# Kernel optimization log

Measured on AMD Instinct MI355X. Metric: run time of the kernel, lower is better.

Reference implementation:

```python
import jax, jax.numpy as jnp
import numpy as np

K_NEIGHBORS = 50
DELTA = 0.001


def setup_inputs() -> dict:
    key = jax.random.key(0)
    k1, k2, k3 = jax.random.split(key, 3)
    A, N, D, B = 8, 50000, 64, 256
    return {
        "query": jax.random.normal(k1, (B, D), dtype=jnp.float32),
        "mem_keys": jax.random.normal(k2, (A, N, D), dtype=jnp.float32),
        "mem_values": jax.random.normal(k3, (A, N), dtype=jnp.float32),
    }


def reference(query, mem_keys, mem_values):
    # query: [B, D]; mem_keys: [A, N, D]; mem_values: [A, N]
    q_sq = jnp.sum(query ** 2, axis=-1, keepdims=True)  # [B, 1]

    def per_action(keys, values):
        # keys: [N, D], values: [N]
        # brute-force squared-L2 distances (replaces Annoy ANN search)
        d2 = q_sq + jnp.sum(keys ** 2, axis=-1)[None, :] - 2.0 * query @ keys.T  # [B, N]
        _, idx = jax.lax.top_k(-d2, K_NEIGHBORS)  # [B, K] nearest indices
        gk = keys[idx]        # [B, K, D] gathered keys
        gv = values[idx]      # [B, K]    gathered values
        # inverse-distance kernel, exact recompute as in torch forward
        dist = jnp.sum((query[:, None, :] - gk) ** 2, axis=-1)  # [B, K]
        w = 1.0 / (dist + DELTA)
        out = jnp.sum(w * gv, axis=-1) / jnp.sum(w, axis=-1)  # [B]
        return out, idx, dist

    vals, idxs, scores = jax.vmap(per_action)(mem_keys, mem_values)  # [A,B], [A,B,K], [A,B,K]
    values_all = vals.T  # [B, A]
    max_values = jnp.max(values_all, axis=-1, keepdims=True)   # [B, 1]
    actions = jnp.argmax(values_all, axis=-1, keepdims=True)   # [B, 1]
    return (max_values, actions, values_all,
            jnp.transpose(idxs, (1, 0, 2)), jnp.transpose(scores, (1, 0, 2)))
```

## Files before the change

kernel.cpp:

```cpp
#include <hip/hip_runtime.h>
#include <cstdint>


#define A_N 8
#define N_N 50000
#define D_N 64
#define B_N 256
#define K_N 50

constexpr int   QT  = 64;
constexpr int   NBT = 128;
constexpr int   NT  = (N_N + NBT - 1) / NBT;
constexpr int   SL  = 56;
constexpr int   SLF = 64;
constexpr int   SLOTS = 20;
constexpr int   CAPMAX = 4096;
constexpr float TMARG = 25.0f;
constexpr int   NPAD = NT * NBT;

constexpr int OFF_MAX = 0;
constexpr int OFF_ACT = 256;
constexpr int OFF_VAL = 512;
constexpr int OFF_IDX = 2560;
constexpr int OFF_SC  = 104960;

constexpr size_t WSF_CNT  = 0;
constexpr size_t WSF_THR  = 8192;
constexpr size_t WSF_KBF  = 1609728;
constexpr size_t WSF_CAND = 52858880;

constexpr size_t WS_CNT  = 0;
constexpr size_t WS_QSQ  = 16384;
constexpr size_t WS_KSQ  = 17408;
constexpr size_t WS_CAND = 1617920;

typedef __attribute__((ext_vector_type(8))) short bf16x8;
typedef __attribute__((ext_vector_type(4))) float f32x4;

__device__ __forceinline__ unsigned bfr(float f)
{
    unsigned u = __float_as_uint(f);
    return (u + 0x7FFFu + ((u >> 16) & 1u)) >> 16;
}
__device__ __forceinline__ uint4 packbf8(const float* f)
{
    uint4 w;
    w.x = bfr(f[0]) | (bfr(f[1]) << 16);
    w.y = bfr(f[2]) | (bfr(f[3]) << 16);
    w.z = bfr(f[4]) | (bfr(f[5]) << 16);
    w.w = bfr(f[6]) | (bfr(f[7]) << 16);
    return w;
}

__device__ __forceinline__ void async16(void* lds, const void* g)
{
    __builtin_amdgcn_global_load_lds(
        (const __attribute__((address_space(1))) void*)g,
        (__attribute__((address_space(3))) void*)lds, 16, 0, 0);
}

__device__ __forceinline__ float np_tree8(const float r[8])
{
    return __fadd_rn(__fadd_rn(__fadd_rn(r[0], r[1]), __fadd_rn(r[2], r[3])),
                     __fadd_rn(__fadd_rn(r[4], r[5]), __fadd_rn(r[6], r[7])));
}

__device__ __forceinline__ float np_sumsq64(const float* __restrict__ a)
{
    float r[8];
#pragma unroll
    for (int j = 0; j < 8; ++j) r[j] = __fmul_rn(a[j], a[j]);
    for (int i = 8; i < 64; i += 8)
#pragma unroll
        for (int j = 0; j < 8; ++j)
            r[j] = __fadd_rn(r[j], __fmul_rn(a[i + j], a[i + j]));
    return np_tree8(r);
}

__device__ __forceinline__ float np_sum50(const float* __restrict__ a)
{
    float r[8];
#pragma unroll
    for (int j = 0; j < 8; ++j) r[j] = a[j];
    for (int i = 8; i < 48; i += 8)
#pragma unroll
        for (int j = 0; j < 8; ++j) r[j] = __fadd_rn(r[j], a[i + j]);
    float res = np_tree8(r);
    res = __fadd_rn(res, a[48]);
    res = __fadd_rn(res, a[49]);
    return res;
}


__global__ __launch_bounds__(256)
void dnd_k0b(const float* __restrict__ keys, float* __restrict__ thrn,
             uint4* __restrict__ kbf, int* __restrict__ cnt)
{
    __shared__ float khalf[NBT][2];
    const int t   = blockIdx.x;
    const int a   = blockIdx.y;
    const int tid = threadIdx.x;
    const int r   = tid >> 1, h = tid & 1;

    int n = t * NBT + r; if (n > N_N - 1) n = N_N - 1;
    const float4* s4 = (const float4*)(keys + ((size_t)a * N_N + n) * D_N + h * 32);
    float4 fv[8];
#pragma unroll
    for (int i = 0; i < 8; ++i) fv[i] = s4[i];
    float ps = 0.f;
#pragma unroll
    for (int i = 0; i < 8; ++i)
        ps += fv[i].x * fv[i].x + fv[i].y * fv[i].y + fv[i].z * fv[i].z + fv[i].w * fv[i].w;
    khalf[r][h] = ps;

    const float* f = (const float*)fv;
    const int s = r >> 4, m = r & 15;
    uint4* dst = kbf + ((size_t)(a * NT + t) * 16 + (s * 2 + h)) * 64;
#pragma unroll
    for (int g = 0; g < 4; ++g) dst[g * 16 + m] = packbf8(f + g * 8);

    __syncthreads();
    if (tid < NBT) {
        const int nn = t * NBT + tid;
        float thr = __builtin_huge_valf();
        if (nn < N_N) {
            const float ks = khalf[tid][0] + khalf[tid][1];
            thr = 0.5f * (ks - TMARG);
        }
        thrn[(size_t)a * NPAD + t * NBT + tid] = thr;
    }
    if (t == 0) cnt[a * B_N + tid] = 0;
}

__global__ __launch_bounds__(256, 7)
void dnd_k1(const float* __restrict__ query, const uint4* __restrict__ kbf,
            const float* __restrict__ thrn,
            int* __restrict__ cnt, unsigned* __restrict__ cand, int cap)
{
    __shared__ __align__(16) uint4 bfrag[16][64];
    __shared__ float    thrs[NBT];
    __shared__ int      lcnt[QT];
    __shared__ unsigned lbuf[QT][SLOTS];

    const int a    = blockIdx.z;
    const int q0   = blockIdx.y * QT;
    const int sl   = blockIdx.x;
    const int tid  = threadIdx.x;
    const int lane = tid & 63;
    const int wave = tid >> 6;
    const int quad = lane >> 4;
    const int nl   = lane & 15;

    bf16x8 aA, aB;
    {
        const float* qb = query + (size_t)(q0 + wave * 16 + nl) * D_N + quad * 8;
        float f0[8], f1[8];
        *(float4*)(f0)     = *(const float4*)(qb);
        *(float4*)(f0 + 4) = *(const float4*)(qb + 4);
        *(float4*)(f1)     = *(const float4*)(qb + 32);
        *(float4*)(f1 + 4) = *(const float4*)(qb + 36);
        uint4 pa = packbf8(f0), pb = packbf8(f1);
        aA = *(bf16x8*)&pa;
        aB = *(bf16x8*)&pb;
    }
    if (tid < QT) lcnt[tid] = 0;

    int it = 0;
    for (int t = sl; t < NT; t += SL, ++it) {
        const int n0 = t * NBT;
        __syncthreads();
        {
            const char* src = (const char*)(kbf + (size_t)(a * NT + t) * 1024);
#pragma unroll
            for (int i = 0; i < 4; ++i) {
                const int off = i * 4096 + tid * 16;
                async16((char*)bfrag + off, src + off);
            }
        }
        if (tid < NBT) thrs[tid] = thrn[(size_t)a * NPAD + n0 + tid];
        __syncthreads();

#pragma unroll
        for (int s = 0; s < 8; ++s) {
            const bf16x8 b0 = ((const bf16x8*)bfrag)[(s * 2 + 0) * 64 + lane];
            const bf16x8 b1 = ((const bf16x8*)bfrag)[(s * 2 + 1) * 64 + lane];
            f32x4 c = {0.f, 0.f, 0.f, 0.f};
            c = __builtin_amdgcn_mfma_f32_16x16x32_bf16(aA, b0, c, 0, 0, 0);
            c = __builtin_amdgcn_mfma_f32_16x16x32_bf16(aB, b1, c, 0, 0, 0);

            const int   nn  = n0 + s * 16 + nl;
            const float thr = thrs[s * 16 + nl];
#pragma unroll
            for (int r = 0; r < 4; ++r) {
                if (c[r] >= thr) {
                    const int bl = wave * 16 + quad * 4 + r;
                    const float d2rel = fmaf(-2.f, c[r], fmaf(2.f, thr, TMARG));
                    int qv = (int)fmaf(d2rel, 1000.f, 40000.f);
                    qv = qv < 0 ? 0 : (qv > 65535 ? 65535 : qv);
                    const unsigned entry = ((unsigned)qv << 16) | (unsigned)nn;
                    const int p = atomicAdd(&lcnt[bl], 1);
                    if (p < SLOTS) lbuf[bl][p] = entry;
                    else {
                        const int gb = a * B_N + q0 + bl;
                        const int gp = atomicAdd(&cnt[gb], 1);
                        if (gp < cap) cand[(size_t)gb * cap + gp] = entry;
                    }
                }
            }
        }

        const bool last = (t + SL >= NT);
        if ((it & 1) || last) {
            __syncthreads();
            if (tid < QT) {
                int m = lcnt[tid]; lcnt[tid] = 0;
                if (m > SLOTS) m = SLOTS;
                if (m > 0) {
                    const int gb = a * B_N + q0 + tid;
                    const int base = atomicAdd(&cnt[gb], m);
                    unsigned* dst = cand + (size_t)gb * cap;
                    for (int i = 0; i < m; ++i) {
                        const int p = base + i;
                        if (p < cap) dst[p] = lbuf[tid][i];
                    }
                }
            }
        }
    }
}

__global__ __launch_bounds__(256)
void dnd_k2(const float* __restrict__ query, const float* __restrict__ keys,
            const float* __restrict__ values,
            const int* __restrict__ cnt, const unsigned* __restrict__ cand, int cap,
            float* __restrict__ dout)
{
    __shared__ __align__(16) float qrow[D_N];
    __shared__ int   hist[256];
    __shared__ float sdf[512];
    __shared__ int   sn[512];
    __shared__ int   wn[K_N];
    __shared__ float wsc[K_N];
    __shared__ float wgv[K_N];
    __shared__ int   nsurv;
    __shared__ int   bstar;
    __shared__ float qsq_np;

    const int b   = blockIdx.x;
    const int a   = blockIdx.y;
    const int ab  = a * B_N + b;
    const int tid = threadIdx.x;

    if (tid < D_N) qrow[tid] = query[(size_t)b * D_N + tid];
    hist[tid & 255] = 0;
    if (tid == 0) nsurv = 0;
    if (tid < K_N) wn[tid] = 0;
    __syncthreads();
    if (tid == 0) qsq_np = np_sumsq64(qrow);
    __syncthreads();

    int c = cnt[ab]; if (c > cap) c = cap;
    const unsigned* base = cand + (size_t)ab * cap;

    for (int i = tid; i < c; i += 256) {
        int bin = (int)(base[i] >> 16) / 250;
        bin = bin > 255 ? 255 : bin;
        atomicAdd(&hist[bin], 1);
    }
    __syncthreads();
    if (tid == 0) {
        const int need = c < K_N ? c : K_N;
        int cum = 0, bs = 255;
        for (int i = 0; i < 256; ++i) { cum += hist[i]; if (cum >= need) { bs = i; break; } }
        bstar = bs;
    }
    __syncthreads();
    const int bs = bstar + 4;

    for (int i = tid; i < c; i += 256) {
        const unsigned e = base[i];
        int bin = (int)(e >> 16) / 250;
        bin = bin > 255 ? 255 : bin;
        if (bin <= bs) {
            int p = atomicAdd(&nsurv, 1);
            if (p < 512) sn[p] = (int)(e & 0xFFFFu);
        }
    }
    __syncthreads();
    int c2 = nsurv; if (c2 > 512) c2 = 512;

    const float qn = qsq_np;
    for (int i = tid; i < c2; i += 256) {
        const int n = sn[i];
        const float4* kr = (const float4*)(keys + ((size_t)a * N_N + n) * D_N);
        const float4* qr = (const float4*)qrow;
        float r[8];
#pragma unroll
    for (int j = 0; j < 8; ++j) r[j] = 0.f;
        float dot = 0.f;
#pragma unroll
        for (int cch = 0; cch < 16; ++cch) {
            float4 kk = kr[cch]; float4 qv = qr[cch];
            const int j0 = (cch & 1) * 4;
            if (cch < 2) {
                r[j0 + 0] = __fmul_rn(kk.x, kk.x);
                r[j0 + 1] = __fmul_rn(kk.y, kk.y);
                r[j0 + 2] = __fmul_rn(kk.z, kk.z);
                r[j0 + 3] = __fmul_rn(kk.w, kk.w);
            } else {
                r[j0 + 0] = __fadd_rn(r[j0 + 0], __fmul_rn(kk.x, kk.x));
                r[j0 + 1] = __fadd_rn(r[j0 + 1], __fmul_rn(kk.y, kk.y));
                r[j0 + 2] = __fadd_rn(r[j0 + 2], __fmul_rn(kk.z, kk.z));
                r[j0 + 3] = __fadd_rn(r[j0 + 3], __fmul_rn(kk.w, kk.w));
            }
            dot = __fmaf_rn(qv.x, kk.x, dot);
            dot = __fmaf_rn(qv.y, kk.y, dot);
            dot = __fmaf_rn(qv.z, kk.z, dot);
            dot = __fmaf_rn(qv.w, kk.w, dot);
        }
        const float ksq = np_tree8(r);
        sdf[i] = __fsub_rn(__fadd_rn(qn, ksq), __fmul_rn(2.0f, dot));
    }
    __syncthreads();

    for (int i = tid; i < c2; i += 256) {
        const float di = sdf[i]; const int ni = sn[i];
        int rank = 0;
        for (int j = 0; j < c2; ++j) {
            const float dj = sdf[j]; const int nj = sn[j];
            rank += (dj < di || (dj == di && nj < ni)) ? 1 : 0;
        }
        if (rank < K_N) wn[rank] = ni;
    }
    __syncthreads();

    if (tid < K_N) {
        const int n = wn[tid];
        const float* kr = keys + ((size_t)a * N_N + n) * D_N;
        float r[8];
#pragma unroll
        for (int j = 0; j < 8; ++j) {
            float d = __fsub_rn(qrow[j], kr[j]);
            r[j] = __fmul_rn(d, d);
        }
        for (int i = 8; i < 64; i += 8)
#pragma unroll
            for (int j = 0; j < 8; ++j) {
                float d = __fsub_rn(qrow[i + j], kr[i + j]);
                r[j] = __fadd_rn(r[j], __fmul_rn(d, d));
            }
        const float dist = np_tree8(r);
        wsc[tid] = dist;
        wgv[tid] = values[(size_t)a * N_N + n];
        dout[OFF_IDX + (size_t)(b * A_N + a) * K_N + tid] = (float)n;
        dout[OFF_SC  + (size_t)(b * A_N + a) * K_N + tid] = dist;
    }
    __syncthreads();

    if (tid == 0) {
        float w[K_N], wv[K_N];
#pragma unroll
        for (int k = 0; k < K_N; ++k) {
            w[k]  = __fdiv_rn(1.0f, __fadd_rn(wsc[k], 0.001f));
            wv[k] = __fmul_rn(w[k], wgv[k]);
        }
        dout[OFF_VAL + b * A_N + a] = __fdiv_rn(np_sum50(wv), np_sum50(w));
    }
}

__global__ void dnd_k3(float* __restrict__ dout)
{
    const int b = threadIdx.x;
    float best = -__builtin_huge_valf(); int bi = 0;
#pragma unroll
    for (int a = 0; a < A_N; ++a) {
        const float v = dout[OFF_VAL + b * A_N + a];
        if (v > best) { best = v; bi = a; }
    }
    dout[OFF_MAX + b] = best;
    dout[OFF_ACT + b] = (float)bi;
}


__global__ __launch_bounds__(256)
void dnd_k0f(const float* __restrict__ query, const float* __restrict__ keys,
             float* __restrict__ qsq_g, float* __restrict__ ksq_g)
{
    const int r = blockIdx.x * 256 + threadIdx.x;
    if (r >= A_N * N_N + B_N) return;
    const bool isk = r < A_N * N_N;
    const float4* s4 = (const float4*)(isk ? (keys + (size_t)r * D_N)
                                           : (query + (size_t)(r - A_N * N_N) * D_N));
    float s = 0.f;
#pragma unroll
    for (int i = 0; i < 16; ++i) {
        float4 v = s4[i];
        s += v.x * v.x + v.y * v.y + v.z * v.z + v.w * v.w;
    }
    if (isk) ksq_g[r] = s; else qsq_g[r - A_N * N_N] = s;
}

__global__ __launch_bounds__(256, 4)
void dnd_k1f(const float* __restrict__ query, const float* __restrict__ keys,
             const float* __restrict__ qsq_g, const float* __restrict__ ksq_g,
             int* __restrict__ cnt, uint2* __restrict__ cand, int cap)
{
    __shared__ __align__(16) uint4 afrag[4][2][64];
    __shared__ __align__(16) uint4 bfrag[8][2][64];
    __shared__ float qsqs[QT];
    __shared__ float ksqs[NBT];

    const int a    = blockIdx.z;
    const int q0   = blockIdx.y * QT;
    const int sl   = blockIdx.x;
    const int tid  = threadIdx.x;
    const int lane = tid & 63;
    const int wave = tid >> 6;
    const int quad = lane >> 4;
    const int nl   = lane & 15;

    {
        const int r = tid & 63, seg = tid >> 6;
        const float4* s4 = (const float4*)(query + (size_t)(q0 + r) * D_N + seg * 16);
        float4 fv[4];
#pragma unroll
        for (int i = 0; i < 4; ++i) fv[i] = s4[i];
        const float* f = (const float*)fv;
        const int qtile = r >> 4, m = r & 15, kh = seg >> 1;
        const int quadA = (seg & 1) * 2;
        afrag[qtile][kh][quadA * 16 + m]       = packbf8(f);
        afrag[qtile][kh][(quadA + 1) * 16 + m] = packbf8(f + 8);
    }
    if (tid < QT) qsqs[tid] = qsq_g[q0 + tid];

    for (int t = sl; t < NT; t += SLF) {
        const int n0 = t * NBT;
        __syncthreads();
        {
            const int r = tid >> 1, h = tid & 1;
            int n = n0 + r; if (n > N_N - 1) n = N_N - 1;
            const float4* s4 = (const float4*)(keys + ((size_t)a * N_N + n) * D_N + h * 32);
            float4 fv[8];
#pragma unroll
            for (int i = 0; i < 8; ++i) fv[i] = s4[i];
            const float* f = (const float*)fv;
            const int s = r >> 4, m = r & 15;
#pragma unroll
            for (int g = 0; g < 4; ++g)
                bfrag[s][h][g * 16 + m] = packbf8(f + g * 8);
        }
        if (tid < NBT)
            ksqs[tid] = (n0 + tid < N_N) ? ksq_g[(size_t)a * N_N + n0 + tid]
                                         : __builtin_huge_valf();
        __syncthreads();

        const bf16x8 aA = ((const bf16x8*)afrag)[(wave * 2 + 0) * 64 + lane];
        const bf16x8 aB = ((const bf16x8*)afrag)[(wave * 2 + 1) * 64 + lane];

#pragma unroll
        for (int s = 0; s < 8; ++s) {
            const bf16x8 b0 = ((const bf16x8*)bfrag)[(s * 2 + 0) * 64 + lane];
            const bf16x8 b1 = ((const bf16x8*)bfrag)[(s * 2 + 1) * 64 + lane];
            f32x4 c = {0.f, 0.f, 0.f, 0.f};
            c = __builtin_amdgcn_mfma_f32_16x16x32_bf16(aA, b0, c, 0, 0, 0);
            c = __builtin_amdgcn_mfma_f32_16x16x32_bf16(aB, b1, c, 0, 0, 0);

            const int   nn  = n0 + s * 16 + nl;
            const float ksq = ksqs[s * 16 + nl];
#pragma unroll
            for (int r = 0; r < 4; ++r) {
                const int   qr = wave * 16 + quad * 4 + r;
                const float qq = qsqs[qr];
                const float d2 = qq + ksq - 2.0f * c[r];
                if (d2 <= qq + TMARG) {
                    const int b = q0 + qr;
                    const int p = atomicAdd(&cnt[a * B_N + b], 1);
                    if (p < cap) {
                        uint2 e; e.x = __float_as_uint(d2); e.y = (unsigned)nn;
                        cand[(size_t)(a * B_N + b) * cap + p] = e;
                    }
                }
            }
        }
    }
}

__global__ __launch_bounds__(256, 2)
void dnd_k2f(const float* __restrict__ query, const float* __restrict__ keys,
             const float* __restrict__ values,
             const int* __restrict__ cnt, const uint2* __restrict__ cand, int cap,
             float* __restrict__ dout)
{
    __shared__ __align__(16) float qrow[D_N];
    __shared__ float cd[CAPMAX];
    __shared__ int   cn[CAPMAX];
    __shared__ int   hist[256];
    __shared__ float sdf[512];
    __shared__ int   sn[512];
    __shared__ int   wn[K_N];
    __shared__ float wsc[K_N];
    __shared__ float wgv[K_N];
    __shared__ int   nsurv;
    __shared__ int   bstar;
    __shared__ float sqsq;
    __shared__ float qsq_np;

    const int b   = blockIdx.x;
    const int a   = blockIdx.y;
    const int ab  = a * B_N + b;
    const int tid = threadIdx.x;

    if (tid < D_N) qrow[tid] = query[(size_t)b * D_N + tid];
    hist[tid & 255] = 0;
    if (tid == 0) nsurv = 0;
    if (tid < K_N) wn[tid] = 0;
    __syncthreads();
    if (tid < 64) {
        float v = qrow[tid];
        float s = v * v;
#pragma unroll
        for (int m = 1; m < 64; m <<= 1) s += __shfl_xor(s, m, 64);
        if (tid == 0) sqsq = s;
    }
    if (tid == 0) qsq_np = np_sumsq64(qrow);
    __syncthreads();

    int c = cnt[ab]; if (c > cap) c = cap; if (c > CAPMAX) c = CAPMAX;
    const float qq = sqsq;

    for (int i = tid; i < c; i += 256) {
        uint2 e = cand[(size_t)ab * cap + i];
        float d = __uint_as_float(e.x);
        cd[i] = d; cn[i] = (int)e.y;
        int bin = (int)((d - qq + 40.f) * 4.f);
        bin = bin < 0 ? 0 : (bin > 255 ? 255 : bin);
        atomicAdd(&hist[bin], 1);
    }
    __syncthreads();
    if (tid == 0) {
        const int need = c < K_N ? c : K_N;
        int cum = 0, bs = 255;
        for (int i = 0; i < 256; ++i) { cum += hist[i]; if (cum >= need) { bs = i; break; } }
        bstar = bs;
    }
    __syncthreads();
    const int bs = bstar + 4;

    for (int i = tid; i < c; i += 256) {
        float d = cd[i];
        int bin = (int)((d - qq + 40.f) * 4.f);
        bin = bin < 0 ? 0 : (bin > 255 ? 255 : bin);
        if (bin <= bs) {
            int p = atomicAdd(&nsurv, 1);
            if (p < 512) sn[p] = cn[i];
        }
    }
    __syncthreads();
    int c2 = nsurv; if (c2 > 512) c2 = 512;

    const float qn = qsq_np;
    for (int i = tid; i < c2; i += 256) {
        const int n = sn[i];
        const float4* kr = (const float4*)(keys + ((size_t)a * N_N + n) * D_N);
        const float4* qr = (const float4*)qrow;
        float r[8];
#pragma unroll
        for (int j = 0; j < 8; ++j) r[j] = 0.f;
        float dot = 0.f;
#pragma unroll
        for (int cch = 0; cch < 16; ++cch) {
            float4 kk = kr[cch]; float4 qv = qr[cch];
            const int j0 = (cch & 1) * 4;
            if (cch < 2) {
                r[j0 + 0] = __fmul_rn(kk.x, kk.x);
                r[j0 + 1] = __fmul_rn(kk.y, kk.y);
                r[j0 + 2] = __fmul_rn(kk.z, kk.z);
                r[j0 + 3] = __fmul_rn(kk.w, kk.w);
            } else {
                r[j0 + 0] = __fadd_rn(r[j0 + 0], __fmul_rn(kk.x, kk.x));
                r[j0 + 1] = __fadd_rn(r[j0 + 1], __fmul_rn(kk.y, kk.y));
                r[j0 + 2] = __fadd_rn(r[j0 + 2], __fmul_rn(kk.z, kk.z));
                r[j0 + 3] = __fadd_rn(r[j0 + 3], __fmul_rn(kk.w, kk.w));
            }
            dot = __fmaf_rn(qv.x, kk.x, dot);
            dot = __fmaf_rn(qv.y, kk.y, dot);
            dot = __fmaf_rn(qv.z, kk.z, dot);
            dot = __fmaf_rn(qv.w, kk.w, dot);
        }
        const float ksq = np_tree8(r);
        sdf[i] = __fsub_rn(__fadd_rn(qn, ksq), __fmul_rn(2.0f, dot));
    }
    __syncthreads();

    for (int i = tid; i < c2; i += 256) {
        const float di = sdf[i]; const int ni = sn[i];
        int rank = 0;
        for (int j = 0; j < c2; ++j) {
            const float dj = sdf[j]; const int nj = sn[j];
            rank += (dj < di || (dj == di && nj < ni)) ? 1 : 0;
        }
        if (rank < K_N) wn[rank] = ni;
    }
    __syncthreads();

    if (tid < K_N) {
        const int n = wn[tid];
        const float* kr = keys + ((size_t)a * N_N + n) * D_N;
        float r[8];
#pragma unroll
        for (int j = 0; j < 8; ++j) {
            float d = __fsub_rn(qrow[j], kr[j]);
            r[j] = __fmul_rn(d, d);
        }
        for (int i = 8; i < 64; i += 8)
#pragma unroll
            for (int j = 0; j < 8; ++j) {
                float d = __fsub_rn(qrow[i + j], kr[i + j]);
                r[j] = __fadd_rn(r[j], __fmul_rn(d, d));
            }
        const float dist = np_tree8(r);
        wsc[tid] = dist;
        wgv[tid] = values[(size_t)a * N_N + n];
        dout[OFF_IDX + (size_t)(b * A_N + a) * K_N + tid] = (float)n;
        dout[OFF_SC  + (size_t)(b * A_N + a) * K_N + tid] = dist;
    }
    __syncthreads();

    if (tid == 0) {
        float w[K_N], wv[K_N];
#pragma unroll
        for (int k = 0; k < K_N; ++k) {
            w[k]  = __fdiv_rn(1.0f, __fadd_rn(wsc[k], 0.001f));
            wv[k] = __fmul_rn(w[k], wgv[k]);
        }
        dout[OFF_VAL + b * A_N + a] = __fdiv_rn(np_sum50(wv), np_sum50(w));
    }
}

extern "C" void kernel_launch(void* const* d_in, const int* in_sizes, int n_in,
                              void* d_out, int out_size, void* d_ws, size_t ws_size,
                              hipStream_t stream)
{
    (void)in_sizes; (void)n_in; (void)out_size;
    const float* query  = (const float*)d_in[0];
    const float* keys   = (const float*)d_in[1];
    const float* values = (const float*)d_in[2];
    float* dout = (float*)d_out;
    char*  ws   = (char*)d_ws;

    long long capf = 0;
    if (ws_size > WSF_CAND)
        capf = (long long)((ws_size - WSF_CAND) / ((size_t)A_N * B_N * 4));
    const bool full = capf >= 3072;

    if (full) {
        int cap = capf > CAPMAX ? CAPMAX : (int)capf;
        int*      cnt  = (int*)(ws + WSF_CNT);
        float*    thrn = (float*)(ws + WSF_THR);
        uint4*    kbf  = (uint4*)(ws + WSF_KBF);
        unsigned* cand = (unsigned*)(ws + WSF_CAND);

        dim3 g0(NT, A_N);
        dnd_k0b<<<g0, 256, 0, stream>>>(keys, thrn, kbf, cnt);
        dim3 g1(SL, 4, A_N);
        dnd_k1<<<g1, 256, 0, stream>>>(query, kbf, thrn, cnt, cand, cap);
        dim3 g2(B_N, A_N);
        dnd_k2<<<g2, 256, 0, stream>>>(query, keys, values, cnt, cand, cap, dout);
        dnd_k3<<<1, 256, 0, stream>>>(dout);
    } else {
        int*   cnt   = (int*)(ws + WS_CNT);
        float* qsq_g = (float*)(ws + WS_QSQ);
        float* ksq_g = (float*)(ws + WS_KSQ);
        uint2* cand  = (uint2*)(ws + WS_CAND);
        int cap = CAPMAX;
        if (ws_size > WS_CAND) {
            size_t avail = (ws_size - WS_CAND) / ((size_t)A_N * B_N * 8);
            if ((size_t)cap > avail) cap = (int)avail;
        }
        if (cap < 1) cap = 1;

        hipMemsetAsync(cnt, 0, A_N * B_N * sizeof(int), stream);
        dnd_k0f<<<(A_N * N_N + B_N + 255) / 256, 256, 0, stream>>>(query, keys, qsq_g, ksq_g);
        dim3 g1(SLF, 4, A_N);
        dnd_k1f<<<g1, 256, 0, stream>>>(query, keys, qsq_g, ksq_g, cnt, cand, cap);
        dim3 g2(B_N, A_N);
        dnd_k2f<<<g2, 256, 0, stream>>>(query, keys, values, cnt, cand, cap, dout);
        dnd_k3<<<1, 256, 0, stream>>>(dout);
    }
}
```

Before: 265.2 us.

## Double-buffer key tiles in the scan kernel with 64-row tiles

The scan kernel now works on 64-row key tiles instead of 128-row tiles, and the preprocessing kernel writes the packed bf16 fragments in that layout. The next tile and its thresholds are prefetched asynchronously into a second LDS buffer while the current tile runs through the MFMA and threshold test, which removes one block-wide barrier per iteration. Local candidate slots are cut from 20 to 12, flushes happen every fourth tile, each wave flushes only its own rows without a barrier, and the occupancy hint goes from 7 to 8 blocks. The risks are more frequent spills of candidates to global atomics, and a possible race if the async copies are not complete when the single barrier is passed.

```diff
diff --git a/kernel.cpp b/kernel.cpp
--- a/kernel.cpp
+++ b/kernel.cpp
@@ -11,9 +11,11 @@
 constexpr int   QT  = 64;
 constexpr int   NBT = 128;
 constexpr int   NT  = (N_N + NBT - 1) / NBT;
-constexpr int   SL  = 56;
+constexpr int   NB64  = 64;
+constexpr int   NT64  = 782;
+constexpr int   SL64  = 64;
 constexpr int   SLF = 64;
-constexpr int   SLOTS = 20;
+constexpr int   SLOTS = 12;
 constexpr int   CAPMAX = 4096;
 constexpr float TMARG = 25.0f;
 constexpr int   NPAD = NT * NBT;
@@ -114,8 +116,10 @@
     khalf[r][h] = ps;
 
     const float* f = (const float*)fv;
-    const int s = r >> 4, m = r & 15;
-    uint4* dst = kbf + ((size_t)(a * NT + t) * 16 + (s * 2 + h)) * 64;
+    const int T  = (t << 1) + (r >> 6);
+    const int rr = r & 63;
+    const int s = rr >> 4, m = rr & 15;
+    uint4* dst = kbf + ((size_t)(a * NT64 + T) * 8 + (s * 2 + h)) * 64;
 #pragma unroll
     for (int g = 0; g < 4; ++g) dst[g * 16 + m] = packbf8(f + g * 8);
 
@@ -132,13 +136,13 @@
     if (t == 0) cnt[a * B_N + tid] = 0;
 }
 
-__global__ __launch_bounds__(256, 7)
+__global__ __launch_bounds__(256, 8)
 void dnd_k1(const float* __restrict__ query, const uint4* __restrict__ kbf,
             const float* __restrict__ thrn,
             int* __restrict__ cnt, unsigned* __restrict__ cand, int cap)
 {
-    __shared__ __align__(16) uint4 bfrag[16][64];
-    __shared__ float    thrs[NBT];
+    __shared__ __align__(16) uint4 bfrag[2][8][64];
+    __shared__ __align__(16) float thrs[2][NB64];
     __shared__ int      lcnt[QT];
     __shared__ unsigned lbuf[QT][SLOTS];
 
@@ -163,33 +167,44 @@
         aA = *(bf16x8*)&pa;
         aB = *(bf16x8*)&pb;
     }
-    if (tid < QT) lcnt[tid] = 0;
-
-    int it = 0;
-    for (int t = sl; t < NT; t += SL, ++it) {
-        const int n0 = t * NBT;
+    if (lane < 16) lcnt[wave * 16 + lane] = 0;
+
+    {
+        const char* src = (const char*)(kbf + (size_t)(a * NT64 + sl) * 512);
+        char* dst = (char*)&bfrag[0][0][0];
+        async16(dst + tid * 16,        src + tid * 16);
+        async16(dst + 4096 + tid * 16, src + 4096 + tid * 16);
+        if (tid < 16)
+            async16((char*)&thrs[0][0] + tid * 16,
+                    (const char*)(thrn + (size_t)a * NPAD + (size_t)sl * NB64) + tid * 16);
+    }
+
+    int it = 0, cur = 0;
+    for (int T = sl; T < NT64; T += SL64, ++it) {
         __syncthreads();
-        {
-            const char* src = (const char*)(kbf + (size_t)(a * NT + t) * 1024);
-#pragma unroll
-            for (int i = 0; i < 4; ++i) {
-                const int off = i * 4096 + tid * 16;
-                async16((char*)bfrag + off, src + off);
-            }
-        }
-        if (tid < NBT) thrs[tid] = thrn[(size_t)a * NPAD + n0 + tid];
-        __syncthreads();
-
-#pragma unroll
-        for (int s = 0; s < 8; ++s) {
-            const bf16x8 b0 = ((const bf16x8*)bfrag)[(s * 2 + 0) * 64 + lane];
-            const bf16x8 b1 = ((const bf16x8*)bfrag)[(s * 2 + 1) * 64 + lane];
+
+        const int Tn = T + SL64;
+        if (Tn < NT64) {
+            const char* src = (const char*)(kbf + (size_t)(a * NT64 + Tn) * 512);
+            char* dst = (char*)&bfrag[cur ^ 1][0][0];
+            async16(dst + tid * 16,        src + tid * 16);
+            async16(dst + 4096 + tid * 16, src + 4096 + tid * 16);
+            if (tid < 16)
+                async16((char*)&thrs[cur ^ 1][0] + tid * 16,
+                        (const char*)(thrn + (size_t)a * NPAD + (size_t)Tn * NB64) + tid * 16);
+        }
+
+        const int n0 = T * NB64;
+#pragma unroll
+        for (int s = 0; s < 4; ++s) {
+            const bf16x8 b0 = ((const bf16x8*)bfrag[cur])[(s * 2 + 0) * 64 + lane];
+            const bf16x8 b1 = ((const bf16x8*)bfrag[cur])[(s * 2 + 1) * 64 + lane];
             f32x4 c = {0.f, 0.f, 0.f, 0.f};
             c = __builtin_amdgcn_mfma_f32_16x16x32_bf16(aA, b0, c, 0, 0, 0);
             c = __builtin_amdgcn_mfma_f32_16x16x32_bf16(aB, b1, c, 0, 0, 0);
 
             const int   nn  = n0 + s * 16 + nl;
-            const float thr = thrs[s * 16 + nl];
+            const float thr = thrs[cur][s * 16 + nl];
 #pragma unroll
             for (int r = 0; r < 4; ++r) {
                 if (c[r] >= thr) {
@@ -209,23 +224,25 @@
             }
         }
 
-        const bool last = (t + SL >= NT);
-        if ((it & 1) || last) {
-            __syncthreads();
-            if (tid < QT) {
-                int m = lcnt[tid]; lcnt[tid] = 0;
-                if (m > SLOTS) m = SLOTS;
+        const bool last = (T + SL64 >= NT64);
+        if ((it & 3) == 3 || last) {
+            if (lane < 16) {
+                const int bl = wave * 16 + lane;
+                int m = lcnt[bl];
                 if (m > 0) {
-                    const int gb = a * B_N + q0 + tid;
+                    lcnt[bl] = 0;
+                    if (m > SLOTS) m = SLOTS;
+                    const int gb = a * B_N + q0 + bl;
                     const int base = atomicAdd(&cnt[gb], m);
                     unsigned* dst = cand + (size_t)gb * cap;
                     for (int i = 0; i < m; ++i) {
                         const int p = base + i;
-                        if (p < cap) dst[p] = lbuf[tid][i];
+                        if (p < cap) dst[p] = lbuf[bl][i];
                     }
                 }
             }
         }
+        cur ^= 1;
     }
 }
 
@@ -296,7 +313,7 @@
         const float4* qr = (const float4*)qrow;
         float r[8];
 #pragma unroll
-    for (int j = 0; j < 8; ++j) r[j] = 0.f;
+        for (int j = 0; j < 8; ++j) r[j] = 0.f;
         float dot = 0.f;
 #pragma unroll
         for (int cch = 0; cch < 16; ++cch) {
@@ -662,7 +679,7 @@
 
         dim3 g0(NT, A_N);
         dnd_k0b<<<g0, 256, 0, stream>>>(keys, thrn, kbf, cnt);
-        dim3 g1(SL, 4, A_N);
+        dim3 g1(SL64, 4, A_N);
         dnd_k1<<<g1, 256, 0, stream>>>(query, kbf, thrn, cnt, cand, cap);
         dim3 g2(B_N, A_N);
         dnd_k2<<<g2, 256, 0, stream>>>(query, keys, values, cnt, cand, cap, dout);
```

After: 268.6 us. Within noise of the previous version (+1.3%).

## Fuse argmax into k2 via completion counter and parallelize serial reductions

Applied to the files above, without the earlier changes.

Removes the separate argmax kernel launch by having the last of the eight action blocks per query, detected with an atomic done counter, compute the max and argmax. It also replaces several single-thread serial steps in k2 with wave-level shuffles: the query squared-norm, the histogram threshold scan (now a parallel prefix scan) and the final weighted sum. Summation order is kept the same as before so results stay bit-exact. The cost is extra atomics and memory-ordering operations, plus a new workspace counter that k0b must zero.

```diff
diff --git a/kernel.cpp b/kernel.cpp
--- a/kernel.cpp
+++ b/kernel.cpp
@@ -25,9 +25,10 @@
 constexpr int OFF_SC  = 104960;
 
 constexpr size_t WSF_CNT  = 0;
-constexpr size_t WSF_THR  = 8192;
-constexpr size_t WSF_KBF  = 1609728;
-constexpr size_t WSF_CAND = 52858880;
+constexpr size_t WSF_DONE = 8192;
+constexpr size_t WSF_THR  = 9216;
+constexpr size_t WSF_KBF  = 1610752;
+constexpr size_t WSF_CAND = 52859904;
 
 constexpr size_t WS_CNT  = 0;
 constexpr size_t WS_QSQ  = 16384;
@@ -59,7 +60,7 @@
         (__attribute__((address_space(3))) void*)lds, 16, 0, 0);
 }
 
-__device__ __forceinline__ float np_tree8(const float r[8])
+__device__ __forceinline__ float np_tree8(const float* r)
 {
     return __fadd_rn(__fadd_rn(__fadd_rn(r[0], r[1]), __fadd_rn(r[2], r[3])),
                      __fadd_rn(__fadd_rn(r[4], r[5]), __fadd_rn(r[6], r[7])));
@@ -94,7 +95,8 @@
 
 __global__ __launch_bounds__(256)
 void dnd_k0b(const float* __restrict__ keys, float* __restrict__ thrn,
-             uint4* __restrict__ kbf, int* __restrict__ cnt)
+             uint4* __restrict__ kbf, int* __restrict__ cnt,
+             int* __restrict__ done)
 {
     __shared__ float khalf[NBT][2];
     const int t   = blockIdx.x;
@@ -130,6 +132,7 @@
         thrn[(size_t)a * NPAD + t * NBT + tid] = thr;
     }
     if (t == 0) cnt[a * B_N + tid] = 0;
+    if (t == 0 && a == 0) done[tid] = 0;
 }
 
 __global__ __launch_bounds__(256, 7)
@@ -233,30 +236,43 @@
 void dnd_k2(const float* __restrict__ query, const float* __restrict__ keys,
             const float* __restrict__ values,
             const int* __restrict__ cnt, const unsigned* __restrict__ cand, int cap,
-            float* __restrict__ dout)
+            int* __restrict__ done, float* __restrict__ dout)
 {
     __shared__ __align__(16) float qrow[D_N];
     __shared__ int   hist[256];
     __shared__ float sdf[512];
     __shared__ int   sn[512];
     __shared__ int   wn[K_N];
-    __shared__ float wsc[K_N];
-    __shared__ float wgv[K_N];
     __shared__ int   nsurv;
     __shared__ int   bstar;
     __shared__ float qsq_np;
 
-    const int b   = blockIdx.x;
-    const int a   = blockIdx.y;
-    const int ab  = a * B_N + b;
-    const int tid = threadIdx.x;
+    const int b    = blockIdx.x;
+    const int a    = blockIdx.y;
+    const int ab   = a * B_N + b;
+    const int tid  = threadIdx.x;
+    const int lane = tid & 63;
 
     if (tid < D_N) qrow[tid] = query[(size_t)b * D_N + tid];
-    hist[tid & 255] = 0;
+    hist[tid] = 0;
     if (tid == 0) nsurv = 0;
     if (tid < K_N) wn[tid] = 0;
-    __syncthreads();
-    if (tid == 0) qsq_np = np_sumsq64(qrow);
+    if (tid < 64) {
+        float rj = 0.f;
+        if (lane < 8) {
+            rj = __fmul_rn(qrow[lane], qrow[lane]);
+#pragma unroll
+            for (int i = 8; i < 64; i += 8)
+                rj = __fadd_rn(rj, __fmul_rn(qrow[i + lane], qrow[i + lane]));
+        }
+        const float r0 = __shfl(rj, 0), r1 = __shfl(rj, 1),
+                    r2 = __shfl(rj, 2), r3 = __shfl(rj, 3),
+                    r4 = __shfl(rj, 4), r5 = __shfl(rj, 5),
+                    r6 = __shfl(rj, 6), r7 = __shfl(rj, 7);
+        if (lane == 0)
+            qsq_np = __fadd_rn(__fadd_rn(__fadd_rn(r0, r1), __fadd_rn(r2, r3)),
+                               __fadd_rn(__fadd_rn(r4, r5), __fadd_rn(r6, r7)));
+    }
     __syncthreads();
 
     int c = cnt[ab]; if (c > cap) c = cap;
@@ -268,11 +284,30 @@
         atomicAdd(&hist[bin], 1);
     }
     __syncthreads();
-    if (tid == 0) {
-        const int need = c < K_N ? c : K_N;
-        int cum = 0, bs = 255;
-        for (int i = 0; i < 256; ++i) { cum += hist[i]; if (cum >= need) { bs = i; break; } }
-        bstar = bs;
+
+    const int need = c < K_N ? c : K_N;
+    if (tid < 64) {
+        const int h0 = hist[tid * 4 + 0], h1 = hist[tid * 4 + 1],
+                  h2 = hist[tid * 4 + 2], h3 = hist[tid * 4 + 3];
+        const int s0 = h0, s1 = s0 + h1, s2 = s1 + h2, s3 = s2 + h3;
+        int pre = s3;
+#pragma unroll
+        for (int m = 1; m < 64; m <<= 1) {
+            const int v = __shfl_up(pre, m, 64);
+            if (lane >= m) pre += v;
+        }
+        const int ex = pre - s3;
+        int cb = 1 << 20;
+        if (ex + s3 >= need)
+            cb = (ex + s0 >= need) ? tid * 4
+               : (ex + s1 >= need) ? tid * 4 + 1
+               : (ex + s2 >= need) ? tid * 4 + 2 : tid * 4 + 3;
+#pragma unroll
+        for (int m = 32; m; m >>= 1) {
+            const int o = __shfl_xor(cb, m, 64);
+            cb = o < cb ? o : cb;
+        }
+        if (lane == 0) bstar = cb;
     }
     __syncthreads();
     const int bs = bstar + 4;
@@ -296,7 +331,7 @@
         const float4* qr = (const float4*)qrow;
         float r[8];
 #pragma unroll
-    for (int j = 0; j < 8; ++j) r[j] = 0.f;
+        for (int j = 0; j < 8; ++j) r[j] = 0.f;
         float dot = 0.f;
 #pragma unroll
         for (int cch = 0; cch < 16; ++cch) {
@@ -334,37 +369,74 @@
     }
     __syncthreads();
 
-    if (tid < K_N) {
-        const int n = wn[tid];
-        const float* kr = keys + ((size_t)a * N_N + n) * D_N;
-        float r[8];
-#pragma unroll
-        for (int j = 0; j < 8; ++j) {
-            float d = __fsub_rn(qrow[j], kr[j]);
-            r[j] = __fmul_rn(d, d);
-        }
-        for (int i = 8; i < 64; i += 8)
+    if (tid < 64) {
+        float dist = 0.f, gv = 0.f;
+        if (lane < K_N) {
+            const int n = wn[lane];
+            const float* kr = keys + ((size_t)a * N_N + n) * D_N;
+            float r[8];
 #pragma unroll
             for (int j = 0; j < 8; ++j) {
-                float d = __fsub_rn(qrow[i + j], kr[i + j]);
-                r[j] = __fadd_rn(r[j], __fmul_rn(d, d));
-            }
-        const float dist = np_tree8(r);
-        wsc[tid] = dist;
-        wgv[tid] = values[(size_t)a * N_N + n];
-        dout[OFF_IDX + (size_t)(b * A_N + a) * K_N + tid] = (float)n;
-        dout[OFF_SC  + (size_t)(b * A_N + a) * K_N + tid] = dist;
-    }
-    __syncthreads();
-
-    if (tid == 0) {
-        float w[K_N], wv[K_N];
-#pragma unroll
-        for (int k = 0; k < K_N; ++k) {
-            w[k]  = __fdiv_rn(1.0f, __fadd_rn(wsc[k], 0.001f));
-            wv[k] = __fmul_rn(w[k], wgv[k]);
-        }
-        dout[OFF_VAL + b * A_N + a] = __fdiv_rn(np_sum50(wv), np_sum50(w));
+                const float d = __fsub_rn(qrow[j], kr[j]);
+                r[j] = __fmul_rn(d, d);
+            }
+            for (int i = 8; i < 64; i += 8)
+#pragma unroll
+                for (int j = 0; j < 8; ++j) {
+                    const float d = __fsub_rn(qrow[i + j], kr[i + j]);
+                    r[j] = __fadd_rn(r[j], __fmul_rn(d, d));
+                }
+            dist = np_tree8(r);
+            gv = values[(size_t)a * N_N + n];
+            dout[OFF_IDX + (size_t)(b * A_N + a) * K_N + lane] = (float)n;
+            dout[OFF_SC  + (size_t)(b * A_N + a) * K_N + lane] = dist;
+        }
+        float w = 0.f, wv = 0.f;
+        if (lane < K_N) {
+            w  = __fdiv_rn(1.0f, __fadd_rn(dist, 0.001f));
+            wv = __fmul_rn(w, gv);
+        }
+        const int j = lane & 7;
+        float rw = __shfl(w, j), rv = __shfl(wv, j);
+#pragma unroll
+        for (int i = 8; i < 48; i += 8) {
+            rw = __fadd_rn(rw, __shfl(w,  i + j));
+            rv = __fadd_rn(rv, __shfl(wv, i + j));
+        }
+        const float w0 = __shfl(rw, 0), w1 = __shfl(rw, 1), w2 = __shfl(rw, 2),
+                    w3 = __shfl(rw, 3), w4 = __shfl(rw, 4), w5 = __shfl(rw, 5),
+                    w6 = __shfl(rw, 6), w7 = __shfl(rw, 7);
+        float sw = __fadd_rn(__fadd_rn(__fadd_rn(w0, w1), __fadd_rn(w2, w3)),
+                             __fadd_rn(__fadd_rn(w4, w5), __fadd_rn(w6, w7)));
+        sw = __fadd_rn(sw, __shfl(w, 48));
+        sw = __fadd_rn(sw, __shfl(w, 49));
+        const float v0 = __shfl(rv, 0), v1 = __shfl(rv, 1), v2 = __shfl(rv, 2),
+                    v3 = __shfl(rv, 3), v4 = __shfl(rv, 4), v5 = __shfl(rv, 5),
+                    v6 = __shfl(rv, 6), v7 = __shfl(rv, 7);
+        float sv = __fadd_rn(__fadd_rn(__fadd_rn(v0, v1), __fadd_rn(v2, v3)),
+                             __fadd_rn(__fadd_rn(v4, v5), __fadd_rn(v6, v7)));
+        sv = __fadd_rn(sv, __shfl(wv, 48));
+        sv = __fadd_rn(sv, __shfl(wv, 49));
+
+        if (lane == 0) {
+            const float val = __fdiv_rn(sv, sw);
+            __hip_atomic_store(&dout[OFF_VAL + b * A_N + a], val,
+                               __ATOMIC_RELEASE, __HIP_MEMORY_SCOPE_AGENT);
+            const int prev = __hip_atomic_fetch_add(&done[b], 1,
+                               __ATOMIC_ACQ_REL, __HIP_MEMORY_SCOPE_AGENT);
+            if (prev == A_N - 1) {
+                float best = -__builtin_huge_valf(); int bi = 0;
+#pragma unroll
+                for (int aa = 0; aa < A_N; ++aa) {
+                    const float v = __hip_atomic_load(
+                        &dout[OFF_VAL + b * A_N + aa],
+                        __ATOMIC_ACQUIRE, __HIP_MEMORY_SCOPE_AGENT);
+                    if (v > best) { best = v; bi = aa; }
+                }
+                dout[OFF_MAX + b] = best;
+                dout[OFF_ACT + b] = (float)bi;
+            }
+        }
     }
 }
 
@@ -656,17 +728,17 @@
     if (full) {
         int cap = capf > CAPMAX ? CAPMAX : (int)capf;
         int*      cnt  = (int*)(ws + WSF_CNT);
+        int*      done = (int*)(ws + WSF_DONE);
         float*    thrn = (float*)(ws + WSF_THR);
         uint4*    kbf  = (uint4*)(ws + WSF_KBF);
         unsigned* cand = (unsigned*)(ws + WSF_CAND);
 
         dim3 g0(NT, A_N);
-        dnd_k0b<<<g0, 256, 0, stream>>>(keys, thrn, kbf, cnt);
+        dnd_k0b<<<g0, 256, 0, stream>>>(keys, thrn, kbf, cnt, done);
         dim3 g1(SL, 4, A_N);
         dnd_k1<<<g1, 256, 0, stream>>>(query, kbf, thrn, cnt, cand, cap);
         dim3 g2(B_N, A_N);
-        dnd_k2<<<g2, 256, 0, stream>>>(query, keys, values, cnt, cand, cap, dout);
-        dnd_k3<<<1, 256, 0, stream>>>(dout);
+        dnd_k2<<<g2, 256, 0, stream>>>(query, keys, values, cnt, cand, cap, done, dout);
     } else {
         int*   cnt   = (int*)(ws + WS_CNT);
         float* qsq_g = (float*)(ws + WS_QSQ);
```

New measurement: 322.1 us. 21.4% more time.
